# Kernel optimization log

Hardware: AMD Instinct MI355X
Metric: run time of the kernel (lower is better)

## Reference

```python
import jax, jax.numpy as jnp
import numpy as np

EMBED_DIM = 768
NUM_HEADS = 12
HEAD_DIM = EMBED_DIM // NUM_HEADS
SCALE = HEAD_DIM ** -0.5


def setup_inputs() -> dict:
    key = jax.random.key(0)
    k1, k2, k3, k4, k5 = jax.random.split(key, 5)
    B, T = 8, 1024
    hidden_states = jax.random.normal(k1, (B, T, EMBED_DIM), dtype=jnp.float32)
    init = 0.02
    qkv_w = jax.random.normal(k2, (EMBED_DIM, 3 * EMBED_DIM), dtype=jnp.float32) * init
    qkv_b = jnp.zeros((3 * EMBED_DIM,), dtype=jnp.float32)
    proj_w = jax.random.normal(k3, (EMBED_DIM, EMBED_DIM), dtype=jnp.float32) * init
    proj_b = jnp.zeros((EMBED_DIM,), dtype=jnp.float32)
    return {
        "hidden_states": hidden_states,
        "qkv_w": qkv_w,
        "qkv_b": qkv_b,
        "proj_w": proj_w,
        "proj_b": proj_b,
    }


def reference(hidden_states, qkv_w, qkv_b, proj_w, proj_b):
    B, T, C = hidden_states.shape
    # fused QKV projection
    mixed = hidden_states @ qkv_w + qkv_b            # [B, T, 3C]
    mixed = mixed.reshape(B, T, 3, NUM_HEADS, HEAD_DIM)
    mixed = jnp.transpose(mixed, (2, 0, 3, 1, 4))    # [3, B, H, T, D]
    q, k, v = mixed[0], mixed[1], mixed[2]
    # scaled dot-product attention (dropout is identity in eval)
    scores = jnp.einsum("bhqd,bhkd->bhqk", q, k) * SCALE
    probs = jax.nn.softmax(scores, axis=-1)
    ctx = jnp.einsum("bhqk,bhkd->bhqd", probs, v)    # [B, H, T, D]
    ctx = jnp.transpose(ctx, (0, 2, 1, 3)).reshape(B, T, C)
    out = ctx @ proj_w + proj_b
    return out
```

## Files before the change

### kernel.cpp

```cpp
#include <hip/hip_runtime.h>

#define EMBED 768
#define NHEAD 12
#define HDIM 64
#define BATCH 8
#define SEQ 1024
#define ROWS (BATCH*SEQ)
#define QKVN (3*EMBED)
#define ATTN_SCALE 0.125f

typedef short s16x8 __attribute__((ext_vector_type(8)));
typedef short s16x4 __attribute__((ext_vector_type(4)));
typedef float f32x4 __attribute__((ext_vector_type(4)));

__device__ __forceinline__ float bf2f(unsigned short u) {
    union { unsigned int i; float f; } v; v.i = ((unsigned int)u) << 16; return v.f;
}
__device__ __forceinline__ unsigned short f2bf(float f) {
    unsigned int i = __builtin_bit_cast(unsigned int, f);
    i += 0x7FFFu + ((i >> 16) & 1u);
    return (unsigned short)(i >> 16);
}

__device__ __forceinline__ void async16(short* lds, const unsigned short* g) {
    __builtin_amdgcn_global_load_lds(
        (const __attribute__((address_space(1))) unsigned int*)g,
        (__attribute__((address_space(3))) unsigned int*)lds,
        16, 0, 0);
}

__device__ __forceinline__ f32x4 mfma16(s16x4 a, s16x4 b, f32x4 c) {
#if __has_builtin(__builtin_amdgcn_mfma_f32_16x16x16bf16_1k)
    return __builtin_amdgcn_mfma_f32_16x16x16bf16_1k(a, b, c, 0, 0, 0);
#else
    asm volatile("v_mfma_f32_16x16x16_bf16 %0, %1, %2, %0" : "+v"(c) : "v"(a), "v"(b));
    return c;
#endif
}

__global__ __launch_bounds__(256) void prep_k(
    const float* __restrict__ qkv_w, unsigned short* __restrict__ WqkvT,
    const float* __restrict__ proj_w, unsigned short* __restrict__ WprojT,
    const float* __restrict__ hidden, unsigned short* __restrict__ hiddenBf)
{
    __shared__ float tile[64][65];
    int blk = blockIdx.x;
    int t = threadIdx.x;
    if (blk < 576) {
        const float* in; unsigned short* outp; int K, N, tx, ty;
        if (blk < 432) { in = qkv_w; outp = WqkvT; K = EMBED; N = QKVN; tx = blk % 36; ty = blk / 36; }
        else { int b2 = blk - 432; in = proj_w; outp = WprojT; K = EMBED; N = EMBED; tx = b2 % 12; ty = b2 / 12; }
        int n0 = tx * 64, k0 = ty * 64;
        int c = t & 63, r0 = t >> 6;
        #pragma unroll
        for (int i = 0; i < 16; i++) {
            int r = r0 * 16 + i;
            tile[r][c] = in[(long long)(k0 + r) * N + n0 + c];
        }
        __syncthreads();
        #pragma unroll
        for (int i = 0; i < 16; i++) {
            int nr = r0 * 16 + i;
            outp[(long long)(n0 + nr) * K + k0 + c] = f2bf(tile[c][nr]);
        }
    } else {
        int tid = (blk - 576) * 256 + t;
        int base = tid * 8;
        float4 f0 = *(const float4*)&hidden[base];
        float4 f1 = *(const float4*)&hidden[base + 4];
        s16x8 a;
        a[0] = (short)f2bf(f0.x); a[1] = (short)f2bf(f0.y);
        a[2] = (short)f2bf(f0.z); a[3] = (short)f2bf(f0.w);
        a[4] = (short)f2bf(f1.x); a[5] = (short)f2bf(f1.y);
        a[6] = (short)f2bf(f1.z); a[7] = (short)f2bf(f1.w);
        *(s16x8*)&hiddenBf[base] = a;
    }
}

template <int OUT_F32>
__global__ __launch_bounds__(256) void gemm128(
    const unsigned short* __restrict__ A,
    const unsigned short* __restrict__ Bt,
    const float* __restrict__ bias,
    void* __restrict__ Cv,
    int M, int N, int K)
{
    __shared__ short As[2][128 * 32];
    __shared__ short Bs[2][128 * 32];
    int t = threadIdx.x, lane = t & 63, w = t >> 6;
    int quad = lane >> 4, low = lane & 15;
    int orig = blockIdx.y * gridDim.x + blockIdx.x;
    int xcd = orig & 7;
    int local = orig >> 3;
    int bx = xcd * 8 + (local & 7);
    int by = local >> 3;
    int m0 = bx * 128, n0 = by * 128;
    int wm = (w & 1) * 64, wn = (w >> 1) * 64;

    int ci0 = w * 128 + lane;
    int r0 = ci0 >> 2, c0 = (ci0 & 3) ^ ((r0 >> 1) & 3);
    int ci1 = ci0 + 64;
    int r1 = ci1 >> 2, c1 = (ci1 & 3) ^ ((r1 >> 1) & 3);
    const unsigned short* pa0 = A + (long long)(m0 + r0) * K + c0 * 8;
    const unsigned short* pa1 = A + (long long)(m0 + r1) * K + c1 * 8;
    const unsigned short* pb0 = Bt + (long long)(n0 + r0) * K + c0 * 8;
    const unsigned short* pb1 = Bt + (long long)(n0 + r1) * K + c1 * 8;
    int lo0 = (w * 128) * 8;
    int lo1 = (w * 128 + 64) * 8;

    async16(&As[0][lo0], pa0);
    async16(&As[0][lo1], pa1);
    async16(&Bs[0][lo0], pb0);
    async16(&Bs[0][lo1], pb1);
    __syncthreads();

    f32x4 acc[4][4] = {};
    int cur = 0;
    for (int k0 = 0; k0 < K; k0 += 32) {
        int nxt = cur ^ 1;
        if (k0 + 32 < K) {
            async16(&As[nxt][lo0], pa0 + k0 + 32);
            async16(&As[nxt][lo1], pa1 + k0 + 32);
            async16(&Bs[nxt][lo0], pb0 + k0 + 32);
            async16(&Bs[nxt][lo1], pb1 + k0 + 32);
        }
        const short* as = As[cur];
        const short* bs = Bs[cur];
        s16x8 af[4], bfr[4];
        #pragma unroll
        for (int i = 0; i < 4; i++) {
            int ra = wm + i * 16 + low;
            af[i] = *(const s16x8*)&as[ra * 32 + ((quad ^ ((ra >> 1) & 3)) * 8)];
            int rb = wn + i * 16 + low;
            bfr[i] = *(const s16x8*)&bs[rb * 32 + ((quad ^ ((rb >> 1) & 3)) * 8)];
        }
        #pragma unroll
        for (int i = 0; i < 4; i++)
            #pragma unroll
            for (int j = 0; j < 4; j++)
                acc[i][j] = __builtin_amdgcn_mfma_f32_16x16x32_bf16(af[i], bfr[j], acc[i][j], 0, 0, 0);
        __syncthreads();
        cur = nxt;
    }
    #pragma unroll
    for (int i = 0; i < 4; i++)
        #pragma unroll
        for (int j = 0; j < 4; j++)
            #pragma unroll
            for (int r = 0; r < 4; r++) {
                int m = m0 + wm + i * 16 + quad * 4 + r;
                int n = n0 + wn + j * 16 + low;
                float v = acc[i][j][r] + bias[n];
                if (OUT_F32) ((float*)Cv)[(long long)m * N + n] = v;
                else ((unsigned short*)Cv)[(long long)m * N + n] = f2bf(v);
            }
}

__global__ __launch_bounds__(512) void attn_k(
    const unsigned short* __restrict__ mixed,
    unsigned short* __restrict__ ctx)
{
    __shared__ __align__(16) char smem[34816];
    int blk = blockIdx.x;
    int bh = blk % 96;
    int qc = blk / 96;
    int b = bh / NHEAD, h = bh - b * NHEAD;
    int t = threadIdx.x;
    int tl = t & 255;
    int lane = t & 63, w = t >> 6;
    int wq = w & 3, gang = w >> 2;
    int quad = lane >> 4, low = lane & 15;
    long long rowbase = (long long)b * SEQ;
    int q0 = qc * 128 + wq * 32;
    int hoff = h * HDIM;

    short* Ks = (short*)(smem + gang * 16896);
    short* Vt = (short*)(smem + gang * 16896 + 8192);

    s16x8 qf[2][2];
    #pragma unroll
    for (int qh = 0; qh < 2; qh++) {
        long long r = (rowbase + q0 + qh * 16 + low) * QKVN + hoff;
        qf[qh][0] = *(const s16x8*)&mixed[r + quad * 8];
        qf[qh][1] = *(const s16x8*)&mixed[r + 32 + quad * 8];
    }

    int s0 = wq * 128 + lane;
    int kr0 = s0 >> 3, kc0 = s0 & 7;
    int kg = kc0 ^ (kr0 & 7);
    const unsigned short* pk0 = mixed + (rowbase + kr0) * QKVN + EMBED + hoff + kg * 8;
    const unsigned short* pk1 = mixed + (rowbase + kr0 + 8) * QKVN + EMBED + hoff + kg * 8;
    short* lk0 = Ks + (wq * 128) * 8;
    short* lk1 = Ks + (wq * 128 + 64) * 8;

    int dblk = tl & 15, rq = tl >> 4;
    const unsigned short* pv = mixed + (rowbase + rq * 4) * QKVN + 2 * EMBED + hoff + dblk * 4;

    f32x4 o[2][4] = {};
    float lsum[2] = {0.f, 0.f};

    int kvbase = gang * 512;
    for (int it = 0; it < 8; it++) {
        long long koff = (long long)(kvbase + it * 64) * QKVN;
        __syncthreads();
        async16(lk0, pk0 + koff);
        async16(lk1, pk1 + koff);
        s16x4 v0 = *(const s16x4*)&pv[koff];
        s16x4 v1 = *(const s16x4*)&pv[koff + QKVN];
        s16x4 v2 = *(const s16x4*)&pv[koff + 2 * QKVN];
        s16x4 v3 = *(const s16x4*)&pv[koff + 3 * QKVN];
        #pragma unroll
        for (int k = 0; k < 4; k++) {
            s16x4 wv;
            wv[0] = v0[k]; wv[1] = v1[k]; wv[2] = v2[k]; wv[3] = v3[k];
            *(s16x4*)&Vt[(dblk * 4 + k) * 68 + rq * 4] = wv;
        }
        __syncthreads();

        f32x4 sT[2][4] = {};
        __builtin_amdgcn_s_setprio(1);
        #pragma unroll
        for (int n = 0; n < 4; n++) {
            int rr = n * 16 + low;
            int key = low & 7;
            s16x8 kf0 = *(const s16x8*)&Ks[rr * 64 + ((quad ^ key) * 8)];
            s16x8 kf1 = *(const s16x8*)&Ks[rr * 64 + (((quad + 4) ^ key) * 8)];
            sT[0][n] = __builtin_amdgcn_mfma_f32_16x16x32_bf16(kf0, qf[0][0], sT[0][n], 0, 0, 0);
            sT[0][n] = __builtin_amdgcn_mfma_f32_16x16x32_bf16(kf1, qf[0][1], sT[0][n], 0, 0, 0);
            sT[1][n] = __builtin_amdgcn_mfma_f32_16x16x32_bf16(kf0, qf[1][0], sT[1][n], 0, 0, 0);
            sT[1][n] = __builtin_amdgcn_mfma_f32_16x16x32_bf16(kf1, qf[1][1], sT[1][n], 0, 0, 0);
        }
        __builtin_amdgcn_s_setprio(0);

        s16x4 pf[2][4];
        #pragma unroll
        for (int qh = 0; qh < 2; qh++)
            #pragma unroll
            for (int n = 0; n < 4; n++) {
                float e0 = __expf(sT[qh][n][0] * ATTN_SCALE);
                float e1 = __expf(sT[qh][n][1] * ATTN_SCALE);
                float e2 = __expf(sT[qh][n][2] * ATTN_SCALE);
                float e3 = __expf(sT[qh][n][3] * ATTN_SCALE);
                lsum[qh] += (e0 + e1) + (e2 + e3);
                unsigned int w0, w1;
                asm("v_cvt_pk_bf16_f32 %0, %1, %2" : "=v"(w0) : "v"(e0), "v"(e1));
                asm("v_cvt_pk_bf16_f32 %0, %1, %2" : "=v"(w1) : "v"(e2), "v"(e3));
                union { unsigned int u[2]; s16x4 v; } pu;
                pu.u[0] = w0; pu.u[1] = w1;
                pf[qh][n] = pu.v;
            }

        __builtin_amdgcn_s_setprio(1);
        #pragma unroll
        for (int nt = 0; nt < 4; nt++) {
            int drow = nt * 16 + low;
            #pragma unroll
            for (int n = 0; n < 4; n++) {
                s16x4 vf = *(const s16x4*)&Vt[drow * 68 + n * 16 + quad * 4];
                o[0][nt] = mfma16(pf[0][n], vf, o[0][nt]);
                o[1][nt] = mfma16(pf[1][n], vf, o[1][nt]);
            }
        }
        __builtin_amdgcn_s_setprio(0);
    }

    #pragma unroll
    for (int qh = 0; qh < 2; qh++) {
        lsum[qh] += __shfl_xor(lsum[qh], 16, 64);
        lsum[qh] += __shfl_xor(lsum[qh], 32, 64);
    }

    f32x4* xo = (f32x4*)smem;
    float*  xl = (float*)(smem + 32768);
    __syncthreads();
    if (gang == 1) {
        #pragma unroll
        for (int qh = 0; qh < 2; qh++) {
            #pragma unroll
            for (int nt = 0; nt < 4; nt++)
                xo[((wq * 2 + qh) * 4 + nt) * 64 + lane] = o[qh][nt];
            xl[(wq * 2 + qh) * 64 + lane] = lsum[qh];
        }
    }
    __syncthreads();
    if (gang == 0) {
        #pragma unroll
        for (int qh = 0; qh < 2; qh++) {
            #pragma unroll
            for (int nt = 0; nt < 4; nt++)
                o[qh][nt] += xo[((wq * 2 + qh) * 4 + nt) * 64 + lane];
            lsum[qh] += xl[(wq * 2 + qh) * 64 + lane];
        }
        #pragma unroll
        for (int qh = 0; qh < 2; qh++)
            #pragma unroll
            for (int r = 0; r < 4; r++) {
                float inv = 1.0f / __shfl(lsum[qh], quad * 4 + r, 64);
                int q = q0 + qh * 16 + quad * 4 + r;
                #pragma unroll
                for (int nt = 0; nt < 4; nt++)
                    ctx[(rowbase + q) * EMBED + hoff + nt * 16 + low] =
                        f2bf(o[qh][nt][r] * inv);
            }
    }
}

extern "C" void kernel_launch(void* const* d_in, const int* in_sizes, int n_in,
                              void* d_out, int out_size, void* d_ws, size_t ws_size,
                              hipStream_t stream) {
    const float* hidden = (const float*)d_in[0];
    const float* qkv_w  = (const float*)d_in[1];
    const float* qkv_b  = (const float*)d_in[2];
    const float* proj_w = (const float*)d_in[3];
    const float* proj_b = (const float*)d_in[4];
    float* out = (float*)d_out;

    char* ws = (char*)d_ws;
    unsigned short* hiddenBf = (unsigned short*)ws;
    unsigned short* ctx      = (unsigned short*)ws;
    unsigned short* WqkvT    = (unsigned short*)(ws + 12582912);
    unsigned short* WprojT   = (unsigned short*)(ws + 16121856);
    unsigned short* mixed    = (unsigned short*)(ws + 17301504);

    prep_k<<<dim3(3648), 256, 0, stream>>>(qkv_w, WqkvT, proj_w, WprojT, hidden, hiddenBf);
    gemm128<0><<<dim3(ROWS / 128, QKVN / 128), 256, 0, stream>>>(
        hiddenBf, WqkvT, qkv_b, mixed, ROWS, QKVN, EMBED);
    attn_k<<<dim3(96 * 8), 512, 0, stream>>>(mixed, ctx);
    gemm128<1><<<dim3(ROWS / 128, EMBED / 128), 256, 0, stream>>>(
        ctx, WprojT, proj_b, out, ROWS, EMBED, EMBED);
}
```

Measured before the change: 190.4 us.

## Double-buffer K tiles and prefetch next V tile during attention compute

Adds a second K shared-memory buffer so the next K/V tile's async loads and V global reads are issued before the current tile's QK and PV MFMAs, overlapping memory latency with compute. V is still single-buffered: it is transposed into shared memory after a barrier at the end of each step. This raises LDS use per block, which may reduce occupancy, and keeps two barriers per iteration.

```diff
diff --git a/kernel.cpp b/kernel.cpp
--- a/kernel.cpp
+++ b/kernel.cpp
@@ -160,7 +160,7 @@
     const unsigned short* __restrict__ mixed,
     unsigned short* __restrict__ ctx)
 {
-    __shared__ __align__(16) char smem[34816];
+    __shared__ __align__(16) char smem[50176];
     int blk = blockIdx.x;
     int bh = blk % 96;
     int qc = blk / 96;
@@ -174,8 +174,9 @@
     int q0 = qc * 128 + wq * 32;
     int hoff = h * HDIM;
 
-    short* Ks = (short*)(smem + gang * 16896);
-    short* Vt = (short*)(smem + gang * 16896 + 8192);
+    short* Ks0 = (short*)(smem + gang * 25088);
+    short* Ks1 = (short*)(smem + gang * 25088 + 8192);
+    short* Vt  = (short*)(smem + gang * 25088 + 16384);
 
     s16x8 qf[2][2];
     #pragma unroll
@@ -190,25 +191,24 @@
     int kg = kc0 ^ (kr0 & 7);
     const unsigned short* pk0 = mixed + (rowbase + kr0) * QKVN + EMBED + hoff + kg * 8;
     const unsigned short* pk1 = mixed + (rowbase + kr0 + 8) * QKVN + EMBED + hoff + kg * 8;
-    short* lk0 = Ks + (wq * 128) * 8;
-    short* lk1 = Ks + (wq * 128 + 64) * 8;
+    int klo0 = (wq * 128) * 8;
+    int klo1 = (wq * 128 + 64) * 8;
 
     int dblk = tl & 15, rq = tl >> 4;
     const unsigned short* pv = mixed + (rowbase + rq * 4) * QKVN + 2 * EMBED + hoff + dblk * 4;
 
     f32x4 o[2][4] = {};
     float lsum[2] = {0.f, 0.f};
-
     int kvbase = gang * 512;
-    for (int it = 0; it < 8; it++) {
-        long long koff = (long long)(kvbase + it * 64) * QKVN;
-        __syncthreads();
-        async16(lk0, pk0 + koff);
-        async16(lk1, pk1 + koff);
-        s16x4 v0 = *(const s16x4*)&pv[koff];
-        s16x4 v1 = *(const s16x4*)&pv[koff + QKVN];
-        s16x4 v2 = *(const s16x4*)&pv[koff + 2 * QKVN];
-        s16x4 v3 = *(const s16x4*)&pv[koff + 3 * QKVN];
+
+    {
+        long long k0off = (long long)kvbase * QKVN;
+        async16(Ks0 + klo0, pk0 + k0off);
+        async16(Ks0 + klo1, pk1 + k0off);
+        s16x4 v0 = *(const s16x4*)&pv[k0off];
+        s16x4 v1 = *(const s16x4*)&pv[k0off + QKVN];
+        s16x4 v2 = *(const s16x4*)&pv[k0off + 2 * QKVN];
+        s16x4 v3 = *(const s16x4*)&pv[k0off + 3 * QKVN];
         #pragma unroll
         for (int k = 0; k < 4; k++) {
             s16x4 wv;
@@ -216,6 +216,20 @@
             *(s16x4*)&Vt[(dblk * 4 + k) * 68 + rq * 4] = wv;
         }
         __syncthreads();
+    }
+
+    auto tile_step = [&](int it, const short* ksCur, short* ksNxt) {
+        bool pf = it < 7;
+        long long koffN = (long long)(kvbase + (it + 1) * 64) * QKVN;
+        s16x4 nv0, nv1, nv2, nv3;
+        if (pf) {
+            async16(ksNxt + klo0, pk0 + koffN);
+            async16(ksNxt + klo1, pk1 + koffN);
+            nv0 = *(const s16x4*)&pv[koffN];
+            nv1 = *(const s16x4*)&pv[koffN + QKVN];
+            nv2 = *(const s16x4*)&pv[koffN + 2 * QKVN];
+            nv3 = *(const s16x4*)&pv[koffN + 3 * QKVN];
+        }
 
         f32x4 sT[2][4] = {};
         __builtin_amdgcn_s_setprio(1);
@@ -223,8 +237,8 @@
         for (int n = 0; n < 4; n++) {
             int rr = n * 16 + low;
             int key = low & 7;
-            s16x8 kf0 = *(const s16x8*)&Ks[rr * 64 + ((quad ^ key) * 8)];
-            s16x8 kf1 = *(const s16x8*)&Ks[rr * 64 + (((quad + 4) ^ key) * 8)];
+            s16x8 kf0 = *(const s16x8*)&ksCur[rr * 64 + ((quad ^ key) * 8)];
+            s16x8 kf1 = *(const s16x8*)&ksCur[rr * 64 + (((quad + 4) ^ key) * 8)];
             sT[0][n] = __builtin_amdgcn_mfma_f32_16x16x32_bf16(kf0, qf[0][0], sT[0][n], 0, 0, 0);
             sT[0][n] = __builtin_amdgcn_mfma_f32_16x16x32_bf16(kf1, qf[0][1], sT[0][n], 0, 0, 0);
             sT[1][n] = __builtin_amdgcn_mfma_f32_16x16x32_bf16(kf0, qf[1][0], sT[1][n], 0, 0, 0);
@@ -232,7 +246,7 @@
         }
         __builtin_amdgcn_s_setprio(0);
 
-        s16x4 pf[2][4];
+        s16x4 pf2[2][4];
         #pragma unroll
         for (int qh = 0; qh < 2; qh++)
             #pragma unroll
@@ -247,7 +261,7 @@
                 asm("v_cvt_pk_bf16_f32 %0, %1, %2" : "=v"(w1) : "v"(e2), "v"(e3));
                 union { unsigned int u[2]; s16x4 v; } pu;
                 pu.u[0] = w0; pu.u[1] = w1;
-                pf[qh][n] = pu.v;
+                pf2[qh][n] = pu.v;
             }
 
         __builtin_amdgcn_s_setprio(1);
@@ -257,11 +271,28 @@
             #pragma unroll
             for (int n = 0; n < 4; n++) {
                 s16x4 vf = *(const s16x4*)&Vt[drow * 68 + n * 16 + quad * 4];
-                o[0][nt] = mfma16(pf[0][n], vf, o[0][nt]);
-                o[1][nt] = mfma16(pf[1][n], vf, o[1][nt]);
+                o[0][nt] = mfma16(pf2[0][n], vf, o[0][nt]);
+                o[1][nt] = mfma16(pf2[1][n], vf, o[1][nt]);
             }
         }
         __builtin_amdgcn_s_setprio(0);
+
+        __syncthreads();
+        if (pf) {
+            #pragma unroll
+            for (int k = 0; k < 4; k++) {
+                s16x4 wv;
+                wv[0] = nv0[k]; wv[1] = nv1[k]; wv[2] = nv2[k]; wv[3] = nv3[k];
+                *(s16x4*)&Vt[(dblk * 4 + k) * 68 + rq * 4] = wv;
+            }
+        }
+        __syncthreads();
+    };
+
+    #pragma unroll 2
+    for (int t2 = 0; t2 < 8; t2 += 2) {
+        tile_step(t2, Ks0, Ks1);
+        tile_step(t2 + 1, Ks1, Ks0);
     }
 
     #pragma unroll
@@ -272,7 +303,6 @@
 
     f32x4* xo = (f32x4*)smem;
     float*  xl = (float*)(smem + 32768);
-    __syncthreads();
     if (gang == 1) {
         #pragma unroll
         for (int qh = 0; qh < 2; qh++) {
```

Result: slower. 199.1 us (+4.6%).
